# Kernel tuning notes

Hardware: AMD Instinct MI355X
Metric: run time of the kernel (lower is better)

Reference implementation:

```python
import jax, jax.numpy as jnp
import numpy as np

EPS = 1e-5

def conv2d(x, w, b=None, pad=1):
    y = jax.lax.conv_general_dilated(x, w, (1, 1), [(pad, pad), (pad, pad)],
                                     dimension_numbers=('NCHW', 'OIHW', 'NCHW'))
    if b is not None:
        y = y + b[None, :, None, None]
    return y

def batchnorm(x, g, b):
    m = x.mean((0, 2, 3), keepdims=True)
    v = x.var((0, 2, 3), keepdims=True)
    return g[None, :, None, None] * (x - m) * jax.lax.rsqrt(v + EPS) + b[None, :, None, None]

def local_conv(x, w12):
    # x: [B,Ci,H,W]; w12: [B,Ci*9,H,W] -> per-pixel depthwise 3x3 conv
    B, Ci, H, W = x.shape
    xp = jnp.pad(x, ((0, 0), (0, 0), (1, 1), (1, 1)))
    patches = jnp.stack([xp[:, :, dh:dh + H, dw:dw + W]
                         for dh in range(3) for dw in range(3)], axis=2)  # [B,Ci,9,H,W]
    return (patches * w12.reshape(B, Ci, 9, H, W)).sum(axis=2)

def setup_inputs() -> dict:
    key = jax.random.key(0)
    ks = jax.random.split(key, 20)
    B, Ci, Cw, H, W = 4, 64, 64, 128, 128
    s = 0.05
    return {
        'input': jax.random.normal(ks[0], (B, Ci, H, W), jnp.float32),
        'weight': jax.random.normal(ks[1], (B, Cw, H, W), jnp.float32),
        'w_conv11': jax.random.normal(ks[2], (Ci, Ci + Cw, 3, 3), jnp.float32) * s,
        'b_conv11': jnp.zeros((Ci,), jnp.float32),
        'w_conv12': jax.random.normal(ks[3], (Ci * 9, Ci, 3, 3), jnp.float32) * s,
        'b_conv12': jnp.zeros((Ci * 9,), jnp.float32),
        'w_conv21': jax.random.normal(ks[4], (Ci, Ci + Cw, 3, 3), jnp.float32) * s,
        'b_conv21': jnp.zeros((Ci,), jnp.float32),
        'w_conv22': jax.random.normal(ks[5], (Ci * Ci, Ci, 1, 1), jnp.float32) * s,
        'b_conv22': jnp.zeros((Ci * Ci,), jnp.float32),
        'local_bn_g': jnp.ones((Ci,), jnp.float32),
        'local_bn_b': jnp.zeros((Ci,), jnp.float32),
        'br_g': jnp.ones((Ci,), jnp.float32),
        'br_b': jnp.zeros((Ci,), jnp.float32),
        'w_conv3': jax.random.normal(ks[6], (Ci, Ci, 3, 3), jnp.float32) * s,
        'conv3_bn_g': jnp.ones((Ci,), jnp.float32),
        'conv3_bn_b': jnp.zeros((Ci,), jnp.float32),
    }

def reference(input, weight, w_conv11, b_conv11, w_conv12, b_conv12,
              w_conv21, b_conv21, w_conv22, b_conv22,
              local_bn_g, local_bn_b, br_g, br_b,
              w_conv3, conv3_bn_g, conv3_bn_b):
    B, Ci, H, W = input.shape
    cat = jnp.concatenate([input, weight], axis=1)
    w11 = jax.nn.relu(conv2d(cat, w_conv11, b_conv11))
    w12 = conv2d(w11, w_conv12, b_conv12)                      # [B,Ci*9,H,W]
    w21 = jax.nn.relu(conv2d(cat, w_conv21, b_conv21))
    pooled = w21.mean((2, 3), keepdims=True)                   # [B,Ci,1,1]
    w22 = conv2d(pooled, w_conv22, b_conv22, pad=0).reshape(B, Ci, Ci)
    out1 = jax.nn.relu(batchnorm(local_conv(input, w12), local_bn_g, local_bn_b))
    out2 = jnp.einsum('bij,bjn->bin', w22, out1.reshape(B, Ci, H * W)).reshape(B, Ci, H, W)
    out3 = jax.nn.relu(batchnorm(out2, br_g, br_b))
    out4 = jax.nn.relu(batchnorm(conv2d(out3, w_conv3, None), conv3_bn_g, conv3_bn_b))
    return out4
```

## Files before the change

### kernel.cpp

```cpp
#include <hip/hip_runtime.h>

#define EPSV 1e-5f
#define HP 130
#define HW 16384

typedef unsigned int u32;
typedef unsigned short bfu;
typedef __bf16 bf16x8 __attribute__((ext_vector_type(8)));
typedef float  f32x4  __attribute__((ext_vector_type(4)));

__device__ __forceinline__ bfu f2bf(float f){
  u32 u = __builtin_bit_cast(u32, f);
  return (bfu)((u + 0x7FFFu + ((u >> 16) & 1u)) >> 16);
}
__device__ __forceinline__ float bf2f(bfu h){
  return __builtin_bit_cast(float, ((u32)h) << 16);
}
__device__ __forceinline__ f32x4 mfma16(bf16x8 a, bf16x8 b, f32x4 c){
  return __builtin_amdgcn_mfma_f32_16x16x32_bf16(a, b, c, 0, 0, 0);
}
__device__ __forceinline__ bf16x8 ldsfrag(const bfu* p){
  return __builtin_bit_cast(bf16x8, *(const uint4*)p);
}
__device__ __forceinline__ void gload_lds16(const uint4* g, uint4* l){
  __builtin_amdgcn_global_load_lds(
      (const __attribute__((address_space(1))) unsigned int*)g,
      (__attribute__((address_space(3))) unsigned int*)l, 16, 0, 0);
}


__global__ void k_zero_border(bfu* catT, bfu* w11T, bfu* out3T){
  int i = blockIdx.x*256 + threadIdx.x;
  if (i >= 4*516) return;
  int b = i/516, r = i - b*516;
  int hp, wpp;
  if (r < 130){ hp = 0; wpp = r; }
  else if (r < 260){ hp = 129; wpp = r - 130; }
  else { int r2 = r - 260; hp = 1 + (r2 >> 1); wpp = (r2 & 1)*129; }
  int pix = (b*HP + hp)*HP + wpp;
  uint4 z = {0,0,0,0};
  uint4* c4 = (uint4*)catT  + (size_t)pix*16;
  uint4* w4 = (uint4*)w11T  + (size_t)pix*8;
  uint4* o4 = (uint4*)out3T + (size_t)pix*8;
  #pragma unroll
  for (int k = 0; k < 16; ++k) c4[k] = z;
  #pragma unroll
  for (int k = 0; k < 8; ++k){ w4[k] = z; o4[k] = z; }
}

__global__ void k_prep_w(const float* __restrict__ w11w, const float* __restrict__ w21w,
                         const float* __restrict__ w12w, const float* __restrict__ w3w,
                         bfu* A11, bfu* A12, bfu* A3){
  const int total = 147456 + 331776 + 36864;
  for (int i = blockIdx.x*256 + threadIdx.x; i < total; i += gridDim.x*256){
    float v; bfu* dst;
    if (i < 147456){
      int tap = i >> 14, och = (i >> 7) & 127, cin = i & 127;
      v = (och < 64) ? w11w[(och*128 + cin)*9 + tap] : w21w[((och-64)*128 + cin)*9 + tap];
      dst = A11 + i;
    } else if (i < 147456 + 331776){
      int i2 = i - 147456;
      int g = i2 >> 12, t = g/9, tap2 = g%9;
      int c = (i2 >> 6) & 63, j = i2 & 63;
      v = w12w[((c*9 + t)*64 + j)*9 + tap2];
      dst = A12 + i2;
    } else {
      int i3 = i - (147456 + 331776);
      int tap2 = i3 >> 12, oc = (i3 >> 6) & 63, j = i3 & 63;
      v = w3w[(oc*64 + j)*9 + tap2];
      dst = A3 + i3;
    }
    *dst = f2bf(v);
  }
}

__global__ void k_prep_cat(const float* __restrict__ inp, const float* __restrict__ wgt, bfu* catT){
  __shared__ bfu lds[128*136];
  int b = blockIdx.y, h = blockIdx.x;
  int t = threadIdx.x;
  int w = t & 127, c0 = t >> 7;
  #pragma unroll 1
  for (int c = c0; c < 128; c += 2){
    const float* src = (c < 64) ? inp + ((b*64 + c)*128 + h)*128
                                : wgt + ((b*64 + (c-64))*128 + h)*128;
    lds[w*136 + c] = f2bf(src[w]);
  }
  __syncthreads();
  uint4* dst = (uint4*)catT;
  #pragma unroll
  for (int k = 0; k < 8; ++k){
    int idx = k*256 + t;
    int pix = idx >> 4, sub = idx & 15;
    uint4 v = *(const uint4*)&lds[pix*136 + sub*8];
    dst[(((b*HP + h+1)*HP) + (pix+1))*16 + sub] = v;
  }
}

__global__ __launch_bounds__(256) void k1_conv(
    const bfu* __restrict__ catT, const bfu* __restrict__ A11,
    const float* __restrict__ b11, const float* __restrict__ b21,
    bfu* __restrict__ w11T, float* __restrict__ poolP){
  __shared__ bfu lds[24480];
  int tid = threadIdx.x;
  int b = blockIdx.y, tile = blockIdx.x;
  int h0 = (tile >> 3)*8, w0 = (tile & 7)*16;

  const uint4* catT4 = (const uint4*)catT;
  for (int s = tid; s < 180*17; s += 256){
    int cell = s/17, sub = s%17;
    if (sub < 16){
      int th = cell/18, tw = cell%18;
      uint4 v = catT4[(((b*HP + h0+th)*HP) + (w0+tw))*16 + sub];
      *(uint4*)&lds[cell*136 + sub*8] = v;
    }
  }
  __syncthreads();

  int wid = tid >> 6, l = tid & 63, lg = l >> 4, pc = l & 15;
  int wm = wid >> 1, wn = wid & 1;
  f32x4 acc[4][4];
  #pragma unroll
  for (int i = 0; i < 4; ++i)
    #pragma unroll
    for (int j = 0; j < 4; ++j) acc[i][j] = f32x4{0.f,0.f,0.f,0.f};

  const uint4* A4 = (const uint4*)A11;
  #pragma unroll 3
  for (int tap = 0; tap < 9; ++tap){
    int kh = tap/3, kw = tap%3;
    #pragma unroll
    for (int jc = 0; jc < 4; ++jc){
      bf16x8 a[4], bb[4];
      #pragma unroll
      for (int fm = 0; fm < 4; ++fm){
        int row = wm*64 + fm*16 + pc;
        a[fm] = __builtin_bit_cast(bf16x8, A4[(tap*128 + row)*16 + jc*4 + lg]);
      }
      #pragma unroll
      for (int fn = 0; fn < 4; ++fn){
        int cell = (wn*4 + fn + kh)*18 + (pc + kw);
        bb[fn] = ldsfrag(&lds[cell*136 + jc*32 + lg*8]);
      }
      #pragma unroll
      for (int fm = 0; fm < 4; ++fm)
        #pragma unroll
        for (int fn = 0; fn < 4; ++fn)
          acc[fm][fn] = mfma16(a[fm], bb[fn], acc[fm][fn]);
    }
  }
  __syncthreads();

  if (wm == 0){
    #pragma unroll
    for (int fm = 0; fm < 4; ++fm)
      #pragma unroll
      for (int r = 0; r < 4; ++r){
        int och = fm*16 + lg*4 + r;
        float bias = b11[och];
        #pragma unroll
        for (int fn = 0; fn < 4; ++fn){
          float v = acc[fm][fn][r] + bias;
          v = v > 0.f ? v : 0.f;
          int px = wn*64 + fn*16 + pc;
          lds[px*72 + och] = f2bf(v);
        }
      }
  } else {
    float* statsF = (float*)&lds[20000];
    #pragma unroll
    for (int fm = 0; fm < 4; ++fm)
      #pragma unroll
      for (int r = 0; r < 4; ++r){
        int cw = fm*16 + lg*4 + r;
        float bias = b21[cw];
        float s = 0.f;
        #pragma unroll
        for (int fn = 0; fn < 4; ++fn){
          float v = acc[fm][fn][r] + bias;
          s += (v > 0.f ? v : 0.f);
        }
        s += __shfl_xor(s,1); s += __shfl_xor(s,2); s += __shfl_xor(s,4); s += __shfl_xor(s,8);
        if (pc == 0) statsF[wn*64 + cw] = s;
      }
  }
  __syncthreads();

  if (wid < 2){
    int px = tid;
    int h = h0 + (px >> 4), w = w0 + (px & 15);
    uint4* dst = (uint4*)w11T + (((b*HP + h+1)*HP) + (w+1))*8;
    const uint4* srcT = (const uint4*)&lds[px*72];
    #pragma unroll
    for (int k = 0; k < 8; ++k) dst[k] = srcT[k];
  }
  if (tid < 64){
    float* statsF = (float*)&lds[20000];
    poolP[(b*128 + tile)*64 + tid] = statsF[tid] + statsF[64 + tid];
  }
}

__global__ void k2a_pool(const float* __restrict__ poolP, float* pooled){
  int t = threadIdx.x;
  int b = t >> 6, c = t & 63;
  float s = 0.f;
  for (int tile = 0; tile < 128; ++tile) s += poolP[(b*128 + tile)*64 + c];
  pooled[t] = s * (1.f/16384.f);
}

__global__ void k2b_w22(const float* __restrict__ pooled, const float* __restrict__ W22,
                        const float* __restrict__ b22, bfu* __restrict__ w22bf){
  __shared__ float pl[64];
  int b = blockIdx.x >> 4, og = blockIdx.x & 15;
  if (threadIdx.x < 64) pl[threadIdx.x] = pooled[b*64 + threadIdx.x];
  __syncthreads();
  int o = og*256 + threadIdx.x;
  float acc = b22[o];
  #pragma unroll 4
  for (int c = 0; c < 64; ++c) acc += pl[c]*W22[o*64 + c];
  w22bf[b*4096 + o] = f2bf(acc);
}

__global__ __launch_bounds__(256) void k3_fused(
    const bfu* __restrict__ w11T, const bfu* __restrict__ catT,
    const bfu* __restrict__ A12, const float* __restrict__ b12,
    float* __restrict__ out1, float* __restrict__ st1){
  __shared__ bfu ldsW[324*64];
  __shared__ bfu ldsA[2*3*4096];
  __shared__ float b12f[576];
  __shared__ float wp[512];
  int tid = threadIdx.x;
  int b = blockIdx.y, tile = blockIdx.x;
  int h0 = (tile >> 3)*16, w0 = (tile & 7)*16;

  int wid = tid >> 6, l = tid & 63, lg = l >> 4, pc = l & 15;
  int w4 = wid*4;

  const uint4* A4 = (const uint4*)A12;
  uint4* ldsA4 = (uint4*)ldsA;
  int srcA = ((tid >> 7)*16 + (tid & 15))*8 + ((tid >> 6) & 1)*4 + ((tid >> 4) & 3);
  uint4* dstBase = ldsA4 + wid*64;

  {
    const uint4* sb = A4 + srcA;
    #pragma unroll
    for (int q = 0; q < 6; ++q)
      gload_lds16(sb + (q>>1)*512 + ((q&1)<<8), dstBase + (q>>1)*512 + ((q&1)<<8));
  }

  const uint4* w11T4 = (const uint4*)w11T;
  for (int s = tid; s < 324*8; s += 256){
    int cell = s >> 3, sub = s & 7;
    int th = cell/18, tw = cell - th*18;
    uint4 v = w11T4[(((b*HP + h0+th)*HP) + (w0+tw))*8 + sub];
    *(uint4*)&ldsW[cell*64 + ((sub*8) ^ ((cell&7)<<3))] = v;
  }
  for (int i = tid; i < 576; i += 256) b12f[i] = b12[i];
  __syncthreads();

  f32x4 oacc[4][4];
  #pragma unroll
  for (int i = 0; i < 4; ++i)
    #pragma unroll
    for (int j = 0; j < 4; ++j) oacc[i][j] = f32x4{0.f,0.f,0.f,0.f};
  f32x4 y[4][4];
  int cur = 0;

  #pragma unroll 1
  for (int cc = 0; cc < 27; ++cc){
    int tt = cc/3, m3 = cc - tt*3;
    if (cc < 26){
      const uint4* sb = A4 + (size_t)((cc+1)*3)*512 + srcA;
      uint4* db = dstBase + (cur^1)*1536;
      #pragma unroll
      for (int q = 0; q < 6; ++q)
        gload_lds16(sb + (q>>1)*512 + ((q&1)<<8), db + (q>>1)*512 + ((q&1)<<8));
    }
    if (m3 == 0){
      #pragma unroll
      for (int i = 0; i < 4; ++i)
        #pragma unroll
        for (int j = 0; j < 4; ++j) y[i][j] = f32x4{0.f,0.f,0.f,0.f};
    }
    #pragma unroll
    for (int t3 = 0; t3 < 3; ++t3){
      #pragma unroll
      for (int jc = 0; jc < 2; ++jc){
        bf16x8 a[4], bbf[4];
        #pragma unroll
        for (int fm = 0; fm < 4; ++fm)
          a[fm] = __builtin_bit_cast(bf16x8, ldsA4[cur*1536 + t3*512 + (fm*2 + jc)*64 + l]);
        #pragma unroll
        for (int fn = 0; fn < 4; ++fn){
          int cell = (w4 + fn + m3)*18 + (pc + t3);
          bbf[fn] = ldsfrag(&ldsW[cell*64 + ((jc*32 + lg*8) ^ ((cell&7)<<3))]);
        }
        #pragma unroll
        for (int fm = 0; fm < 4; ++fm)
          #pragma unroll
          for (int fn = 0; fn < 4; ++fn)
            y[fm][fn] = mfma16(a[fm], bbf[fn], y[fm][fn]);
      }
    }
    __syncthreads();
    if (m3 == 2){
      int dh = tt/3, dw = tt - dh*3;
      #pragma unroll
      for (int fn = 0; fn < 4; ++fn){
        const bfu* base = catT + ((size_t)((b*HP + h0 + w4 + fn + dh)*HP) + (w0 + pc + dw))*128 + lg*4;
        #pragma unroll
        for (int fm = 0; fm < 4; ++fm){
          ushort4 iv = *(const ushort4*)(base + fm*16);
          float i0 = bf2f(iv.x), i1 = bf2f(iv.y), i2 = bf2f(iv.z), i3 = bf2f(iv.w);
          int c = fm*16 + lg*4;
          oacc[fm][fn][0] += i0 * (y[fm][fn][0] + b12f[(c+0)*9 + tt]);
          oacc[fm][fn][1] += i1 * (y[fm][fn][1] + b12f[(c+1)*9 + tt]);
          oacc[fm][fn][2] += i2 * (y[fm][fn][2] + b12f[(c+2)*9 + tt]);
          oacc[fm][fn][3] += i3 * (y[fm][fn][3] + b12f[(c+3)*9 + tt]);
        }
      }
    }
    cur ^= 1;
  }

  #pragma unroll
  for (int fm = 0; fm < 4; ++fm)
    #pragma unroll
    for (int r = 0; r < 4; ++r){
      int c = fm*16 + lg*4 + r;
      float s = 0.f, ss = 0.f;
      #pragma unroll
      for (int fn = 0; fn < 4; ++fn){
        float v = oacc[fm][fn][r];
        out1[((b*64 + c)*128 + h0 + w4 + fn)*128 + (w0 + pc)] = v;
        s += v; ss += v*v;
      }
      s += __shfl_xor(s,1); s += __shfl_xor(s,2); s += __shfl_xor(s,4); s += __shfl_xor(s,8);
      ss += __shfl_xor(ss,1); ss += __shfl_xor(ss,2); ss += __shfl_xor(ss,4); ss += __shfl_xor(ss,8);
      if (pc == 0){ wp[(wid*64 + c)*2] = s; wp[(wid*64 + c)*2 + 1] = ss; }
    }
  __syncthreads();
  if (tid < 64){
    float s = 0.f, ss = 0.f;
    #pragma unroll
    for (int w = 0; w < 4; ++w){ s += wp[(w*64 + tid)*2]; ss += wp[(w*64 + tid)*2 + 1]; }
    int blin = b*64 + tile;
    st1[(blin*64 + tid)*2] = s; st1[(blin*64 + tid)*2 + 1] = ss;
  }
}

__global__ void k_bnstat(const float* __restrict__ st, int nblk, float n,
                         const float* __restrict__ g, const float* __restrict__ bb, float* bn){
  __shared__ float red[512];
  int tid = threadIdx.x;
  int c = tid & 63, kk = tid >> 6;
  float s = 0.f, ss = 0.f;
  for (int k = kk; k < nblk; k += 4){
    float2 v = *(const float2*)&st[(k*64 + c)*2];
    s += v.x; ss += v.y;
  }
  red[tid*2] = s; red[tid*2 + 1] = ss;
  __syncthreads();
  if (tid < 64){
    #pragma unroll
    for (int q = 1; q < 4; ++q){ s += red[(q*64 + tid)*2]; ss += red[(q*64 + tid)*2 + 1]; }
    float mean = s/n, var = ss/n - mean*mean;
    float a = g[tid]*rsqrtf(var + EPSV);
    bn[tid*2] = a; bn[tid*2 + 1] = bb[tid] - mean*a;
  }
}

__global__ __launch_bounds__(256) void k4_einsum(
    const float* __restrict__ out1, const bfu* __restrict__ w22bf,
    const float* __restrict__ bn1, float* __restrict__ out2, float* __restrict__ st2){
  __shared__ bfu ldsX[256*72];
  __shared__ float a1[64], be1[64];
  __shared__ float wp[512];
  int tid = threadIdx.x;
  int b = blockIdx.y, chunk = blockIdx.x;
  if (tid < 64){ a1[tid] = bn1[tid*2]; be1[tid] = bn1[tid*2 + 1]; }
  __syncthreads();
  int p0 = chunk*256;

  {
    int px = tid;
    const float* src = out1 + (size_t)(b*64)*HW + p0 + px;
    #pragma unroll 1
    for (int j0 = 0; j0 < 64; j0 += 4){
      float x0 = src[(j0+0)*HW]; x0 = a1[j0+0]*x0 + be1[j0+0]; x0 = x0 > 0.f ? x0 : 0.f;
      float x1 = src[(j0+1)*HW]; x1 = a1[j0+1]*x1 + be1[j0+1]; x1 = x1 > 0.f ? x1 : 0.f;
      float x2 = src[(j0+2)*HW]; x2 = a1[j0+2]*x2 + be1[j0+2]; x2 = x2 > 0.f ? x2 : 0.f;
      float x3 = src[(j0+3)*HW]; x3 = a1[j0+3]*x3 + be1[j0+3]; x3 = x3 > 0.f ? x3 : 0.f;
      ushort4 pk; pk.x = f2bf(x0); pk.y = f2bf(x1); pk.z = f2bf(x2); pk.w = f2bf(x3);
      *(ushort4*)&ldsX[px*72 + j0] = pk;
    }
  }
  __syncthreads();

  int wid = tid >> 6, l = tid & 63, lg = l >> 4, pc = l & 15;
  const uint4* W4 = (const uint4*)w22bf;
  f32x4 acc[4][4];
  #pragma unroll
  for (int i = 0; i < 4; ++i)
    #pragma unroll
    for (int j = 0; j < 4; ++j) acc[i][j] = f32x4{0.f,0.f,0.f,0.f};

  #pragma unroll
  for (int jc = 0; jc < 2; ++jc){
    bf16x8 a[4], bb[4];
    #pragma unroll
    for (int fm = 0; fm < 4; ++fm)
      a[fm] = __builtin_bit_cast(bf16x8, W4[b*512 + (fm*16 + pc)*8 + jc*4 + lg]);
    #pragma unroll
    for (int fn = 0; fn < 4; ++fn)
      bb[fn] = ldsfrag(&ldsX[(wid*64 + fn*16 + pc)*72 + jc*32 + lg*8]);
    #pragma unroll
    for (int fm = 0; fm < 4; ++fm)
      #pragma unroll
      for (int fn = 0; fn < 4; ++fn)
        acc[fm][fn] = mfma16(a[fm], bb[fn], acc[fm][fn]);
  }

  #pragma unroll
  for (int fm = 0; fm < 4; ++fm)
    #pragma unroll
    for (int r = 0; r < 4; ++r){
      int i = fm*16 + lg*4 + r;
      float s = 0.f, ss = 0.f;
      #pragma unroll
      for (int fn = 0; fn < 4; ++fn){
        int px = wid*64 + fn*16 + pc;
        float v = acc[fm][fn][r];
        out2[(b*64 + i)*HW + p0 + px] = v;
        s += v; ss += v*v;
      }
      s += __shfl_xor(s,1); s += __shfl_xor(s,2); s += __shfl_xor(s,4); s += __shfl_xor(s,8);
      ss += __shfl_xor(ss,1); ss += __shfl_xor(ss,2); ss += __shfl_xor(ss,4); ss += __shfl_xor(ss,8);
      if (pc == 0){ wp[(wid*64 + i)*2] = s; wp[(wid*64 + i)*2 + 1] = ss; }
    }
  __syncthreads();
  if (tid < 64){
    float s = 0.f, ss = 0.f;
    #pragma unroll
    for (int w = 0; w < 4; ++w){ s += wp[(w*64 + tid)*2]; ss += wp[(w*64 + tid)*2 + 1]; }
    int blin = b*64 + chunk;
    st2[(blin*64 + tid)*2] = s; st2[(blin*64 + tid)*2 + 1] = ss;
  }
}

__global__ void k4c_out3(const float* __restrict__ out2, const float* __restrict__ bn2, bfu* out3T){
  __shared__ bfu lds[128*72];
  int b = blockIdx.y, h = blockIdx.x;
  int t = threadIdx.x;
  int px = t & 127, ch = (t >> 7)*32;
  #pragma unroll 1
  for (int cc = 0; cc < 32; cc += 4){
    int c = ch + cc;
    float x0 = out2[((b*64 + c+0) << 14) + (h << 7) + px];
    float x1 = out2[((b*64 + c+1) << 14) + (h << 7) + px];
    float x2 = out2[((b*64 + c+2) << 14) + (h << 7) + px];
    float x3 = out2[((b*64 + c+3) << 14) + (h << 7) + px];
    x0 = bn2[(c+0)*2]*x0 + bn2[(c+0)*2+1]; x0 = x0 > 0.f ? x0 : 0.f;
    x1 = bn2[(c+1)*2]*x1 + bn2[(c+1)*2+1]; x1 = x1 > 0.f ? x1 : 0.f;
    x2 = bn2[(c+2)*2]*x2 + bn2[(c+2)*2+1]; x2 = x2 > 0.f ? x2 : 0.f;
    x3 = bn2[(c+3)*2]*x3 + bn2[(c+3)*2+1]; x3 = x3 > 0.f ? x3 : 0.f;
    ushort4 pk; pk.x = f2bf(x0); pk.y = f2bf(x1); pk.z = f2bf(x2); pk.w = f2bf(x3);
    *(ushort4*)&lds[px*72 + c] = pk;
  }
  __syncthreads();
  uint4* dst = (uint4*)out3T;
  #pragma unroll
  for (int k = 0; k < 4; ++k){
    int idx = k*256 + t;
    int pix = idx >> 3, sub = idx & 7;
    uint4 v = *(const uint4*)&lds[pix*72 + sub*8];
    dst[((size_t)(b*HP + h+1)*HP + (pix+1))*8 + sub] = v;
  }
}

__global__ __launch_bounds__(256) void k5_conv3(
    const bfu* __restrict__ out3T, const bfu* __restrict__ A3,
    float* __restrict__ outc, float* __restrict__ st3){
  __shared__ bfu lds[180*72];
  __shared__ float wp[512];
  int tid = threadIdx.x;
  int b = blockIdx.y, tile = blockIdx.x;
  int h0 = (tile >> 3)*8, w0 = (tile & 7)*16;
  const uint4* src4 = (const uint4*)out3T;
  for (int s = tid; s < 180*8; s += 256){
    int cell = s >> 3, sub = s & 7;
    int th = cell/18, tw = cell - th*18;
    *(uint4*)&lds[cell*72 + sub*8] = src4[(((b*HP + h0+th)*HP) + (w0+tw))*8 + sub];
  }
  __syncthreads();

  int wid = tid >> 6, l = tid & 63, lg = l >> 4, pc = l & 15;
  f32x4 acc[4][2];
  #pragma unroll
  for (int i = 0; i < 4; ++i){ acc[i][0] = f32x4{0.f,0.f,0.f,0.f}; acc[i][1] = f32x4{0.f,0.f,0.f,0.f}; }
  const uint4* A4 = (const uint4*)A3;
  #pragma unroll 3
  for (int tap2 = 0; tap2 < 9; ++tap2){
    int kh = tap2/3, kw = tap2 - kh*3;
    #pragma unroll
    for (int jc = 0; jc < 2; ++jc){
      bf16x8 a[4], bb[2];
      #pragma unroll
      for (int fm = 0; fm < 4; ++fm)
        a[fm] = __builtin_bit_cast(bf16x8, A4[tap2*512 + (fm*16 + pc)*8 + jc*4 + lg]);
      #pragma unroll
      for (int fn = 0; fn < 2; ++fn){
        int cell = (wid*2 + fn + kh)*18 + (pc + kw);
        bb[fn] = ldsfrag(&lds[cell*72 + jc*32 + lg*8]);
      }
      #pragma unroll
      for (int fm = 0; fm < 4; ++fm)
        #pragma unroll
        for (int fn = 0; fn < 2; ++fn)
          acc[fm][fn] = mfma16(a[fm], bb[fn], acc[fm][fn]);
    }
  }
  #pragma unroll
  for (int fm = 0; fm < 4; ++fm)
    #pragma unroll
    for (int r = 0; r < 4; ++r){
      int c = fm*16 + lg*4 + r;
      float s = 0.f, ss = 0.f;
      #pragma unroll
      for (int fn = 0; fn < 2; ++fn){
        int pr = wid*2 + fn;
        float v = acc[fm][fn][r];
        outc[((b*64 + c)*128 + h0 + pr)*128 + (w0 + pc)] = v;
        s += v; ss += v*v;
      }
      s += __shfl_xor(s,1); s += __shfl_xor(s,2); s += __shfl_xor(s,4); s += __shfl_xor(s,8);
      ss += __shfl_xor(ss,1); ss += __shfl_xor(ss,2); ss += __shfl_xor(ss,4); ss += __shfl_xor(ss,8);
      if (pc == 0){ wp[(wid*64 + c)*2] = s; wp[(wid*64 + c)*2 + 1] = ss; }
    }
  __syncthreads();
  if (tid < 64){
    float s = 0.f, ss = 0.f;
    #pragma unroll
    for (int w = 0; w < 4; ++w){ s += wp[(w*64 + tid)*2]; ss += wp[(w*64 + tid)*2 + 1]; }
    int blin = b*128 + tile;
    st3[(blin*64 + tid)*2] = s; st3[(blin*64 + tid)*2 + 1] = ss;
  }
}

__global__ void k6_final(float4* __restrict__ out, const float* __restrict__ bn3){
  const int total4 = 4*64*HW/4;
  for (int i = blockIdx.x*256 + threadIdx.x; i < total4; i += gridDim.x*256){
    int c = (i >> 12) & 63;
    float a = bn3[c*2], be = bn3[c*2 + 1];
    float4 x = out[i];
    x.x = a*x.x + be; x.x = x.x > 0.f ? x.x : 0.f;
    x.y = a*x.y + be; x.y = x.y > 0.f ? x.y : 0.f;
    x.z = a*x.z + be; x.z = x.z > 0.f ? x.z : 0.f;
    x.w = a*x.w + be; x.w = x.w > 0.f ? x.w : 0.f;
    out[i] = x;
  }
}

extern "C" void kernel_launch(void* const* d_in, const int* in_sizes, int n_in,
                              void* d_out, int out_size, void* d_ws, size_t ws_size,
                              hipStream_t stream){
  const float* inp  = (const float*)d_in[0];
  const float* wgt  = (const float*)d_in[1];
  const float* w11w = (const float*)d_in[2];
  const float* b11  = (const float*)d_in[3];
  const float* w12w = (const float*)d_in[4];
  const float* b12  = (const float*)d_in[5];
  const float* w21w = (const float*)d_in[6];
  const float* b21  = (const float*)d_in[7];
  const float* W22  = (const float*)d_in[8];
  const float* b22  = (const float*)d_in[9];
  const float* lg   = (const float*)d_in[10];
  const float* lb   = (const float*)d_in[11];
  const float* brg  = (const float*)d_in[12];
  const float* brb  = (const float*)d_in[13];
  const float* w3w  = (const float*)d_in[14];
  const float* c3g  = (const float*)d_in[15];
  const float* c3b  = (const float*)d_in[16];

  if (ws_size < 53200000) return;

  char* ws = (char*)d_ws;
  bfu*   catT  = (bfu*)(ws);
  bfu*   w11T  = (bfu*)(ws + 17305600);
  bfu*   out3T = (bfu*)(ws + 25958400);
  bfu*   A11   = (bfu*)(ws + 34611200);
  bfu*   A12   = (bfu*)(ws + 34906112);
  bfu*   A3    = (bfu*)(ws + 35569664);
  float* out1  = (float*)(ws + 35643392);
  float* poolP = (float*)(ws + 52420608);
  float* pooled= (float*)(ws + 52551680);
  bfu*   w22bf = (bfu*)(ws + 52552704);
  float* st13  = (float*)(ws + 52585472);
  float* bn1   = (float*)(ws + 52847616);
  float* st2   = (float*)(ws + 52848128);
  float* bn2   = (float*)(ws + 52979200);
  float* bn3   = (float*)(ws + 52979712);
  float* outF  = (float*)d_out;

  k_zero_border<<<dim3(9),  dim3(256), 0, stream>>>(catT, w11T, out3T);
  k_prep_w  <<<dim3(512),  dim3(256), 0, stream>>>(w11w, w21w, w12w, w3w, A11, A12, A3);
  k_prep_cat<<<dim3(128,4),dim3(256), 0, stream>>>(inp, wgt, catT);
  k1_conv   <<<dim3(128,4),dim3(256), 0, stream>>>(catT, A11, b11, b21, w11T, poolP);
  k2a_pool  <<<dim3(1),    dim3(256), 0, stream>>>(poolP, pooled);
  k2b_w22   <<<dim3(64),   dim3(256), 0, stream>>>(pooled, W22, b22, w22bf);
  k3_fused  <<<dim3(64,4), dim3(256), 0, stream>>>(w11T, catT, A12, b12, out1, st13);
  k_bnstat  <<<dim3(1),    dim3(256), 0, stream>>>(st13, 256, 65536.f, lg, lb, bn1);
  k4_einsum <<<dim3(64,4), dim3(256), 0, stream>>>(out1, w22bf, bn1, outF, st2);
  k_bnstat  <<<dim3(1),    dim3(256), 0, stream>>>(st2, 256, 65536.f, brg, brb, bn2);
  k4c_out3  <<<dim3(128,4),dim3(256), 0, stream>>>(outF, bn2, out3T);
  k5_conv3  <<<dim3(128,4),dim3(256), 0, stream>>>(out3T, A3, outF, st13);
  k_bnstat  <<<dim3(1),    dim3(256), 0, stream>>>(st13, 512, 65536.f, c3g, c3b, bn3);
  k6_final  <<<dim3(1024), dim3(256), 0, stream>>>((float4*)outF, bn3);
}
```

Measured before the change: 284.2 us.

## Split k3 tap reduction across two block groups and compute BN stats separately

The fused local-conv kernel now splits its 9-tap conv12 weight-chunk loop across a new grid z dimension: one group handles 5 taps, the other 4. Each group writes its own partial output, to out1 or to the output buffer. The per-stage LDS A buffer is cut to a single tap, which lowers LDS use. A new reduction kernel sums the two partials to produce BN statistics, and the einsum kernel adds the partials when it loads them. The aim is to double block count and occupancy on the main GEMM-like kernel. The cost is writing and re-reading an extra 16 MB partial tensor plus one more launch.

```diff
diff --git a/kernel.cpp b/kernel.cpp
--- a/kernel.cpp
+++ b/kernel.cpp
@@ -223,14 +223,16 @@
 __global__ __launch_bounds__(256) void k3_fused(
     const bfu* __restrict__ w11T, const bfu* __restrict__ catT,
     const bfu* __restrict__ A12, const float* __restrict__ b12,
-    float* __restrict__ out1, float* __restrict__ st1){
+    float* __restrict__ out1, float* __restrict__ outP){
   __shared__ bfu ldsW[324*64];
-  __shared__ bfu ldsA[2*3*4096];
+  __shared__ bfu ldsA[2*4096];
   __shared__ float b12f[576];
-  __shared__ float wp[512];
   int tid = threadIdx.x;
-  int b = blockIdx.y, tile = blockIdx.x;
+  int b = blockIdx.y, tile = blockIdx.x, g = blockIdx.z;
   int h0 = (tile >> 3)*16, w0 = (tile & 7)*16;
+  int base = g ? 5 : 0;
+  int ns   = g ? 4 : 5;
+  float* outp = g ? outP : out1;
 
   int wid = tid >> 6, l = tid & 63, lg = l >> 4, pc = l & 15;
   int w4 = wid*4;
@@ -241,10 +243,9 @@
   uint4* dstBase = ldsA4 + wid*64;
 
   {
-    const uint4* sb = A4 + srcA;
-    #pragma unroll
-    for (int q = 0; q < 6; ++q)
-      gload_lds16(sb + (q>>1)*512 + ((q&1)<<8), dstBase + (q>>1)*512 + ((q&1)<<8));
+    const uint4* sb = A4 + (size_t)base*512 + srcA;
+    gload_lds16(sb,       dstBase);
+    gload_lds16(sb + 256, dstBase + 256);
   }
 
   const uint4* w11T4 = (const uint4*)w11T;
@@ -263,62 +264,70 @@
     #pragma unroll
     for (int j = 0; j < 4; ++j) oacc[i][j] = f32x4{0.f,0.f,0.f,0.f};
   f32x4 y[4][4];
-  int cur = 0;
+  int cur = 0, tt = 0, s = 0;
+  const int NQ = ns*9;
 
   #pragma unroll 1
-  for (int cc = 0; cc < 27; ++cc){
-    int tt = cc/3, m3 = cc - tt*3;
-    if (cc < 26){
-      const uint4* sb = A4 + (size_t)((cc+1)*3)*512 + srcA;
-      uint4* db = dstBase + (cur^1)*1536;
-      #pragma unroll
-      for (int q = 0; q < 6; ++q)
-        gload_lds16(sb + (q>>1)*512 + ((q&1)<<8), db + (q>>1)*512 + ((q&1)<<8));
-    }
-    if (m3 == 0){
+  for (int q = 0; q < NQ; ++q){
+    if (q + 1 < NQ){
+      int s1 = s + 1, tt1 = tt;
+      if (s1 == ns){ s1 = 0; ++tt1; }
+      const uint4* sb = A4 + (size_t)(tt1*9 + base + s1)*512 + srcA;
+      uint4* db = ldsA4 + (cur^1)*512 + wid*64;
+      gload_lds16(sb,       db);
+      gload_lds16(sb + 256, db + 256);
+    }
+    if (s == 0){
       #pragma unroll
       for (int i = 0; i < 4; ++i)
         #pragma unroll
         for (int j = 0; j < 4; ++j) y[i][j] = f32x4{0.f,0.f,0.f,0.f};
     }
-    #pragma unroll
-    for (int t3 = 0; t3 < 3; ++t3){
-      #pragma unroll
-      for (int jc = 0; jc < 2; ++jc){
-        bf16x8 a[4], bbf[4];
+    int tap2 = base + s;
+    int kh = (tap2 >= 6) ? 2 : ((tap2 >= 3) ? 1 : 0);
+    int kw = tap2 - kh*3;
+    #pragma unroll
+    for (int jc = 0; jc < 2; ++jc){
+      bf16x8 a[4], bbf[4];
+      #pragma unroll
+      for (int fm = 0; fm < 4; ++fm)
+        a[fm] = __builtin_bit_cast(bf16x8, ldsA4[cur*512 + (fm*2 + jc)*64 + l]);
+      #pragma unroll
+      for (int fn = 0; fn < 4; ++fn){
+        int cell = (w4 + fn + kh)*18 + (pc + kw);
+        bbf[fn] = ldsfrag(&ldsW[cell*64 + ((jc*32 + lg*8) ^ ((cell&7)<<3))]);
+      }
+      #pragma unroll
+      for (int fm = 0; fm < 4; ++fm)
         #pragma unroll
-        for (int fm = 0; fm < 4; ++fm)
-          a[fm] = __builtin_bit_cast(bf16x8, ldsA4[cur*1536 + t3*512 + (fm*2 + jc)*64 + l]);
-        #pragma unroll
-        for (int fn = 0; fn < 4; ++fn){
-          int cell = (w4 + fn + m3)*18 + (pc + t3);
-          bbf[fn] = ldsfrag(&ldsW[cell*64 + ((jc*32 + lg*8) ^ ((cell&7)<<3))]);
-        }
-        #pragma unroll
-        for (int fm = 0; fm < 4; ++fm)
-          #pragma unroll
-          for (int fn = 0; fn < 4; ++fn)
-            y[fm][fn] = mfma16(a[fm], bbf[fn], y[fm][fn]);
-      }
+        for (int fn = 0; fn < 4; ++fn)
+          y[fm][fn] = mfma16(a[fm], bbf[fn], y[fm][fn]);
     }
     __syncthreads();
-    if (m3 == 2){
-      int dh = tt/3, dw = tt - dh*3;
+
+    if (s == ns - 1){
+      int dh = (tt >= 6) ? 2 : ((tt >= 3) ? 1 : 0);
+      int dw = tt - dh*3;
       #pragma unroll
       for (int fn = 0; fn < 4; ++fn){
-        const bfu* base = catT + ((size_t)((b*HP + h0 + w4 + fn + dh)*HP) + (w0 + pc + dw))*128 + lg*4;
+        const bfu* bp = catT + ((size_t)((b*HP + h0 + w4 + fn + dh)*HP) + (w0 + pc + dw))*128 + lg*4;
         #pragma unroll
         for (int fm = 0; fm < 4; ++fm){
-          ushort4 iv = *(const ushort4*)(base + fm*16);
+          ushort4 iv = *(const ushort4*)(bp + fm*16);
           float i0 = bf2f(iv.x), i1 = bf2f(iv.y), i2 = bf2f(iv.z), i3 = bf2f(iv.w);
           int c = fm*16 + lg*4;
-          oacc[fm][fn][0] += i0 * (y[fm][fn][0] + b12f[(c+0)*9 + tt]);
-          oacc[fm][fn][1] += i1 * (y[fm][fn][1] + b12f[(c+1)*9 + tt]);
-          oacc[fm][fn][2] += i2 * (y[fm][fn][2] + b12f[(c+2)*9 + tt]);
-          oacc[fm][fn][3] += i3 * (y[fm][fn][3] + b12f[(c+3)*9 + tt]);
+          float bz0 = g ? 0.f : b12f[(c+0)*9 + tt];
+          float bz1 = g ? 0.f : b12f[(c+1)*9 + tt];
+          float bz2 = g ? 0.f : b12f[(c+2)*9 + tt];
+          float bz3 = g ? 0.f : b12f[(c+3)*9 + tt];
+          oacc[fm][fn][0] += i0 * (y[fm][fn][0] + bz0);
+          oacc[fm][fn][1] += i1 * (y[fm][fn][1] + bz1);
+          oacc[fm][fn][2] += i2 * (y[fm][fn][2] + bz2);
+          oacc[fm][fn][3] += i3 * (y[fm][fn][3] + bz3);
         }
       }
     }
+    ++s; if (s == ns){ s = 0; ++tt; }
     cur ^= 1;
   }
 
@@ -327,24 +336,34 @@
     #pragma unroll
     for (int r = 0; r < 4; ++r){
       int c = fm*16 + lg*4 + r;
-      float s = 0.f, ss = 0.f;
-      #pragma unroll
-      for (int fn = 0; fn < 4; ++fn){
-        float v = oacc[fm][fn][r];
-        out1[((b*64 + c)*128 + h0 + w4 + fn)*128 + (w0 + pc)] = v;
-        s += v; ss += v*v;
-      }
-      s += __shfl_xor(s,1); s += __shfl_xor(s,2); s += __shfl_xor(s,4); s += __shfl_xor(s,8);
-      ss += __shfl_xor(ss,1); ss += __shfl_xor(ss,2); ss += __shfl_xor(ss,4); ss += __shfl_xor(ss,8);
-      if (pc == 0){ wp[(wid*64 + c)*2] = s; wp[(wid*64 + c)*2 + 1] = ss; }
-    }
-  __syncthreads();
-  if (tid < 64){
-    float s = 0.f, ss = 0.f;
-    #pragma unroll
-    for (int w = 0; w < 4; ++w){ s += wp[(w*64 + tid)*2]; ss += wp[(w*64 + tid)*2 + 1]; }
-    int blin = b*64 + tile;
-    st1[(blin*64 + tid)*2] = s; st1[(blin*64 + tid)*2 + 1] = ss;
+      #pragma unroll
+      for (int fn = 0; fn < 4; ++fn)
+        outp[((b*64 + c)*128 + h0 + w4 + fn)*128 + (w0 + pc)] = oacc[fm][fn][r];
+    }
+}
+
+__global__ __launch_bounds__(256) void k3b_stat(
+    const float* __restrict__ out1, const float* __restrict__ outP, float* __restrict__ st){
+  __shared__ float red[8];
+  int bc = blockIdx.x, t = threadIdx.x;
+  const float4* p1 = (const float4*)(out1 + (size_t)bc*HW);
+  const float4* p2 = (const float4*)(outP + (size_t)bc*HW);
+  float s = 0.f, ss = 0.f;
+  #pragma unroll 4
+  for (int i = t; i < 4096; i += 256){
+    float4 a = p1[i], q = p2[i];
+    float v0 = a.x+q.x, v1 = a.y+q.y, v2 = a.z+q.z, v3 = a.w+q.w;
+    s  += v0+v1+v2+v3;
+    ss += v0*v0+v1*v1+v2*v2+v3*v3;
+  }
+  #pragma unroll
+  for (int m = 1; m < 64; m <<= 1){ s += __shfl_xor(s, m); ss += __shfl_xor(ss, m); }
+  if ((t & 63) == 0){ red[(t >> 6)*2] = s; red[(t >> 6)*2 + 1] = ss; }
+  __syncthreads();
+  if (t == 0){
+    s  = red[0] + red[2] + red[4] + red[6];
+    ss = red[1] + red[3] + red[5] + red[7];
+    st[bc*2] = s; st[bc*2 + 1] = ss;
   }
 }
 
@@ -370,8 +389,9 @@
 }
 
 __global__ __launch_bounds__(256) void k4_einsum(
-    const float* __restrict__ out1, const bfu* __restrict__ w22bf,
-    const float* __restrict__ bn1, float* __restrict__ out2, float* __restrict__ st2){
+    const float* __restrict__ out1, const float* __restrict__ outP,
+    const bfu* __restrict__ w22bf, const float* __restrict__ bn1,
+    float* __restrict__ out2, float* __restrict__ st2){
   __shared__ bfu ldsX[256*72];
   __shared__ float a1[64], be1[64];
   __shared__ float wp[512];
@@ -383,13 +403,14 @@
 
   {
     int px = tid;
-    const float* src = out1 + (size_t)(b*64)*HW + p0 + px;
+    const float* src1 = out1 + (size_t)(b*64)*HW + p0 + px;
+    const float* src2 = outP + (size_t)(b*64)*HW + p0 + px;
     #pragma unroll 1
     for (int j0 = 0; j0 < 64; j0 += 4){
-      float x0 = src[(j0+0)*HW]; x0 = a1[j0+0]*x0 + be1[j0+0]; x0 = x0 > 0.f ? x0 : 0.f;
-      float x1 = src[(j0+1)*HW]; x1 = a1[j0+1]*x1 + be1[j0+1]; x1 = x1 > 0.f ? x1 : 0.f;
-      float x2 = src[(j0+2)*HW]; x2 = a1[j0+2]*x2 + be1[j0+2]; x2 = x2 > 0.f ? x2 : 0.f;
-      float x3 = src[(j0+3)*HW]; x3 = a1[j0+3]*x3 + be1[j0+3]; x3 = x3 > 0.f ? x3 : 0.f;
+      float x0 = src1[(j0+0)*HW] + src2[(j0+0)*HW]; x0 = a1[j0+0]*x0 + be1[j0+0]; x0 = x0 > 0.f ? x0 : 0.f;
+      float x1 = src1[(j0+1)*HW] + src2[(j0+1)*HW]; x1 = a1[j0+1]*x1 + be1[j0+1]; x1 = x1 > 0.f ? x1 : 0.f;
+      float x2 = src1[(j0+2)*HW] + src2[(j0+2)*HW]; x2 = a1[j0+2]*x2 + be1[j0+2]; x2 = x2 > 0.f ? x2 : 0.f;
+      float x3 = src1[(j0+3)*HW] + src2[(j0+3)*HW]; x3 = a1[j0+3]*x3 + be1[j0+3]; x3 = x3 > 0.f ? x3 : 0.f;
       ushort4 pk; pk.x = f2bf(x0); pk.y = f2bf(x1); pk.z = f2bf(x2); pk.w = f2bf(x3);
       *(ushort4*)&ldsX[px*72 + j0] = pk;
     }
@@ -607,9 +628,10 @@
   k1_conv   <<<dim3(128,4),dim3(256), 0, stream>>>(catT, A11, b11, b21, w11T, poolP);
   k2a_pool  <<<dim3(1),    dim3(256), 0, stream>>>(poolP, pooled);
   k2b_w22   <<<dim3(64),   dim3(256), 0, stream>>>(pooled, W22, b22, w22bf);
-  k3_fused  <<<dim3(64,4), dim3(256), 0, stream>>>(w11T, catT, A12, b12, out1, st13);
-  k_bnstat  <<<dim3(1),    dim3(256), 0, stream>>>(st13, 256, 65536.f, lg, lb, bn1);
-  k4_einsum <<<dim3(64,4), dim3(256), 0, stream>>>(out1, w22bf, bn1, outF, st2);
+  k3_fused  <<<dim3(64,4,2),dim3(256),0, stream>>>(w11T, catT, A12, b12, out1, outF);
+  k3b_stat  <<<dim3(256),  dim3(256), 0, stream>>>(out1, outF, st13);
+  k_bnstat  <<<dim3(1),    dim3(256), 0, stream>>>(st13, 4, 65536.f, lg, lb, bn1);
+  k4_einsum <<<dim3(64,4), dim3(256), 0, stream>>>(out1, outF, w22bf, bn1, outF, st2);
   k_bnstat  <<<dim3(1),    dim3(256), 0, stream>>>(st2, 256, 65536.f, brg, brb, bn2);
   k4c_out3  <<<dim3(128,4),dim3(256), 0, stream>>>(outF, bn2, out3T);
   k5_conv3  <<<dim3(128,4),dim3(256), 0, stream>>>(out3T, A3, outF, st13);
```

Result: slower. 321.4 us (+13.1%).
